# Performance work log

Hardware: AMD Instinct MI355X
Metric: run time of the kernel (lower is better)

The kernel has to match this reference:

```python
import jax, jax.numpy as jnp
import numpy as np

L_ITERS = 8   # number of ReduNet layers
C = 10        # number of classes
D = 1024      # feature dimension
N = 4096      # number of samples (columns of Z)


def setup_inputs() -> dict:
    key = jax.random.key(0)
    k0, k1, k2, k3 = jax.random.split(key, 4)
    Z = jax.random.normal(k0, (D, N), dtype=jnp.float32)
    # column-normalized features, as the net maintains at every layer
    Z = Z / jnp.linalg.norm(Z, axis=0, keepdims=True)
    # Elist[l]: (D,D) expansion operator; Cslist[l]: (C,D,D) per-class compression operators
    Elist = jax.random.normal(k1, (L_ITERS, D, D), dtype=jnp.float32) / np.float32(np.sqrt(D))
    Cslist = jax.random.normal(k2, (L_ITERS, C, D, D), dtype=jnp.float32) / np.float32(np.sqrt(D))
    gamma = jax.random.uniform(k3, (C,), dtype=jnp.float32)
    gamma = gamma / jnp.sum(gamma)
    eta = jnp.asarray(0.5, dtype=jnp.float32)
    temperature = jnp.asarray(0.1, dtype=jnp.float32)
    return {"Z": Z, "Elist": Elist, "Cslist": Cslist, "gamma": gamma,
            "eta": eta, "temperature": temperature, "L": L_ITERS}


def reference(Z, Elist, Cslist, gamma, eta, temperature, L):
    for l in range(L):
        Cs = Cslist[l]                                   # (C, d, d)
        CZ = jnp.einsum('cij,jn->cin', Cs, Z)            # (C, d, n)
        sims = -jnp.sqrt(jnp.sum(CZ * CZ, axis=1))       # fro norm over dim=1 -> (C, n)
        P_hat = jax.nn.softmax(sims / temperature, axis=0)  # softmax over classes
        PZ = P_hat[:, None, :] * Z                       # (C, d, n)
        term = jnp.einsum('c,cij,cjn->in', gamma, Cs, PZ)   # gamma-weighted class compression
        grads = Elist[l] @ Z - term                      # (d, n)
        Z = Z + eta * grads
        Z = Z / jnp.linalg.norm(Z, axis=0, keepdims=True)   # column-wise normalization
    return Z
```

## Files before the change

### kernel.cpp

```cpp
#include <hip/hip_runtime.h>
#include <hip/hip_bf16.h>
#include <stdint.h>

#define D_DIM 1024
#define N_DIM 4096
#define C_CLS 10
#define L_IT 8
#define M_DIM 11264
#define NBM 44

typedef __bf16 bf16_t;
typedef __bf16 bf16x8 __attribute__((ext_vector_type(8)));
typedef __bf16 bf16x4 __attribute__((ext_vector_type(4)));
typedef float  f32x4  __attribute__((ext_vector_type(4)));
typedef unsigned short u16x8 __attribute__((ext_vector_type(8)));

__device__ __forceinline__ float bf2f(uint16_t u) {
  union { uint32_t i; float f; } x; x.i = ((uint32_t)u) << 16; return x.f;
}

__global__ __launch_bounds__(256) void pack_w(const float4* __restrict__ Cs,
                                              const float4* __restrict__ El,
                                              bf16x4* __restrict__ dst) {
  const int CS4 = C_CLS * D_DIM * D_DIM / 4;
  int i = blockIdx.x * 256 + threadIdx.x;
  float4 v = (i < CS4) ? Cs[i] : El[i - CS4];
  bf16x4 o;
  o[0] = (bf16_t)v.x; o[1] = (bf16_t)v.y; o[2] = (bf16_t)v.z; o[3] = (bf16_t)v.w;
  dst[i] = o;
}

__global__ __launch_bounds__(256) void init_zt(const float* __restrict__ Zin,
                                               float* __restrict__ ZfT,
                                               bf16_t* __restrict__ ZbT) {
  __shared__ float tile[32][33];
  int tx = threadIdx.x & 31, ty = threadIdx.x >> 5;
  int nb = blockIdx.x, db = blockIdx.y;
  int n = nb * 32 + tx;
#pragma unroll
  for (int j = 0; j < 32; j += 8) {
    int d = db * 32 + ty + j;
    tile[ty + j][tx] = Zin[(size_t)d * N_DIM + n];
  }
  __syncthreads();
  int d2 = db * 32 + tx;
#pragma unroll
  for (int j = 0; j < 32; j += 8) {
    int n2 = nb * 32 + ty + j;
    float v = tile[tx][ty + j];
    ZfT[(size_t)n2 * D_DIM + d2] = v;
    ZbT[(size_t)n2 * D_DIM + d2] = (bf16_t)v;
  }
}

__global__ __launch_bounds__(256) void final_out(const float* __restrict__ ZfT,
                                                 float* __restrict__ outp) {
  __shared__ float tile[32][33];
  int tx = threadIdx.x & 31, ty = threadIdx.x >> 5;
  int nb = blockIdx.x, db = blockIdx.y;
#pragma unroll
  for (int j = 0; j < 32; j += 8) {
    int n = nb * 32 + ty + j;
    int d = db * 32 + tx;
    tile[ty + j][tx] = ZfT[(size_t)n * D_DIM + d];
  }
  __syncthreads();
#pragma unroll
  for (int j = 0; j < 32; j += 8) {
    int d2 = db * 32 + ty + j;
    int n2 = nb * 32 + tx;
    outp[(size_t)d2 * N_DIM + n2] = tile[tx][ty + j];
  }
}


#define SA(buf, h, t) do {                                                              \
    _Pragma("unroll") for (int e_ = 0; e_ < 2; ++e_) {                                  \
      const bf16_t* s_ = Wb + aoff0[e_] + (size_t)(h) * 65536 + (size_t)(t) * 64;       \
      __builtin_amdgcn_global_load_lds(                                                 \
        (const __attribute__((address_space(1))) void*)s_,                              \
        (__attribute__((address_space(3))) void*)(lds + (buf)*16384 + (h)*8192 + dstslot[e_]), \
        16, 0, 0);                                                                      \
    } } while (0)

#define SBst(buf, h, t) do {                                                            \
    _Pragma("unroll") for (int e_ = 0; e_ < 2; ++e_) {                                  \
      const bf16_t* s_ = ZbT + boff0[e_] + (size_t)(h) * 32768 + (size_t)(t) * 64;      \
      __builtin_amdgcn_global_load_lds(                                                 \
        (const __attribute__((address_space(1))) void*)s_,                              \
        (__attribute__((address_space(3))) void*)(lds + 32768 + (buf)*16384 + (h)*8192 + dstslot[e_]), \
        16, 0, 0);                                                                      \
    } } while (0)

#define LOAD_A(buf, qm) do {                                                            \
    _Pragma("unroll") for (int f_ = 0; f_ < 4; ++f_)                                    \
      _Pragma("unroll") for (int kk_ = 0; kk_ < 2; ++kk_)                               \
        a[f_][kk_] = *(const bf16x8*)(lds + (buf)*16384 + (qm)*8192 + aRowBase + f_*1024 + sidx[kk_]); \
  } while (0)

#define LOAD_Bq(buf, qn, arr) do {                                                      \
    _Pragma("unroll") for (int f_ = 0; f_ < 2; ++f_)                                    \
      _Pragma("unroll") for (int kk_ = 0; kk_ < 2; ++kk_)                               \
        arr[f_][kk_] = *(const bf16x8*)(lds + 32768 + (buf)*16384 + (qn)*8192 + bRowBase + f_*1024 + sidx[kk_]); \
  } while (0)

#define MFMAQ(qm, qn, arr) do {                                                         \
    _Pragma("unroll") for (int mm_ = 0; mm_ < 4; ++mm_)                                 \
      _Pragma("unroll") for (int nn_ = 0; nn_ < 2; ++nn_)                               \
        _Pragma("unroll") for (int kk_ = 0; kk_ < 2; ++kk_)                             \
          acc[(qm)*4+mm_][(qn)*2+nn_] = __builtin_amdgcn_mfma_f32_16x16x32_bf16(        \
            a[mm_][kk_], arr[nn_][kk_], acc[(qm)*4+mm_][(qn)*2+nn_], 0, 0, 0);          \
  } while (0)

#define BAR   __builtin_amdgcn_s_barrier()
#define VM(n) asm volatile("s_waitcnt vmcnt(" #n ")" ::: "memory")
#define PRIO1 __builtin_amdgcn_s_setprio(1)
#define PRIO0 __builtin_amdgcn_s_setprio(0)

#define PH(qm, LOADS, STAGES, WAIT) do {                                                \
    LOADS;                                                                              \
    STAGES;                                                                             \
    BAR;                                                                                \
    PRIO1;                                                                              \
    MFMAQ(qm, 0, b0);                                                                   \
    MFMAQ(qm, 1, b1);                                                                   \
    PRIO0;                                                                              \
    WAIT;                                                                               \
    BAR;                                                                                \
  } while (0)

__global__ __launch_bounds__(512, 2) void gemm_wz8(const bf16_t* __restrict__ Wb,
                                                   const bf16_t* __restrict__ ZbT,
                                                   bf16_t* __restrict__ OUT_T, int ldn,
                                                   float* __restrict__ ssq) {
  __shared__ __align__(16) bf16_t lds[65536];

  int nwg = gridDim.x;
  int bid = blockIdx.x;
  int q = nwg >> 3, r = nwg & 7;
  int xcd = bid & 7, idx = bid >> 3;
  int swz = (xcd < r ? xcd * (q + 1) : r * (q + 1) + (xcd - r) * q) + idx;
  int bm = swz % NBM, bn = swz / NBM;
  int m0 = bm * 256, n0 = bn * 256;

  int tid = threadIdx.x;
  int wave = tid >> 6, lane = tid & 63;
  int wrow = wave >> 2, wcol = wave & 3;
  int lm = lane & 15, lks = lane >> 4;
  int sw = lm & 7;

  size_t aoff0[2], boff0[2];
  int dstslot[2];
#pragma unroll
  for (int e = 0; e < 2; ++e) {
    int j = e * 512 + tid;
    int rih = j >> 3, sl = j & 7;
    int sg = sl ^ (rih & 7);
    int arow = (rih & 63) + ((rih >> 6) << 7);
    int brow = (rih & 31) + ((rih >> 5) << 6);
    aoff0[e] = (size_t)(m0 + arow) * 1024 + sg * 8;
    boff0[e] = (size_t)(n0 + brow) * 1024 + sg * 8;
    dstslot[e] = e * 4096 + wave * 512;
  }

  int aRowBase = (wrow * 64 + lm) * 64;
  int bRowBase = (wcol * 32 + lm) * 64;
  int sidx[2] = { ((0 + lks) ^ sw) * 8, ((4 + lks) ^ sw) * 8 };

  f32x4 acc[8][4] = {};
  bf16x8 a[4][2], b0[2][2], b1[2][2];

  SA(0, 0, 0); SBst(0, 0, 0); SBst(0, 1, 0);
  SA(0, 1, 0);
  SA(1, 0, 1); SBst(1, 0, 1); SBst(1, 1, 1);
  VM(8);
  BAR;

  for (int it = 0; it < 8; ++it) {
    int tO = 2 * it + 1, tN = 2 * it + 2, tM = 2 * it + 3;
    bool st = (it < 7);

    PH(0,
       LOAD_A(0, 0); LOAD_Bq(0, 0, b0); LOAD_Bq(0, 1, b1),
       SA(1, 1, tO),
       VM(8));

    if (st) {
      PH(1, LOAD_A(0, 1), SA(0, 0, tN); SBst(0, 0, tN); SBst(0, 1, tN), VM(8));
    } else {
      PH(1, LOAD_A(0, 1), , VM(2));
    }

    if (st) {
      PH(0, LOAD_A(1, 0); LOAD_Bq(1, 0, b0); LOAD_Bq(1, 1, b1), SA(0, 1, tN), VM(8));
    } else {
      PH(0, LOAD_A(1, 0); LOAD_Bq(1, 0, b0); LOAD_Bq(1, 1, b1), , VM(0));
    }

    if (st) {
      PH(1, LOAD_A(1, 1), SA(1, 0, tM); SBst(1, 0, tM); SBst(1, 1, tM), VM(8));
    } else {
      PH(1, LOAD_A(1, 1), , );
    }
  }

#pragma unroll
  for (int mf = 0; mf < 8; ++mf)
#pragma unroll
    for (int nf = 0; nf < 4; ++nf) {
      int col = n0 + wcol * 64 + nf * 16 + lm;
      int row = m0 + wrow * 128 + mf * 16 + lks * 4;
      bf16x4 v;
#pragma unroll
      for (int rr = 0; rr < 4; ++rr) v[rr] = (bf16_t)acc[mf][nf][rr];
      *(bf16x4*)(OUT_T + (size_t)col * M_DIM + row) = v;
    }

  if (m0 < C_CLS * 1024) {
    int c = m0 >> 10;
#pragma unroll
    for (int nf = 0; nf < 4; ++nf) {
      float v = 0.f;
#pragma unroll
      for (int mf = 0; mf < 8; ++mf)
#pragma unroll
        for (int rr = 0; rr < 4; ++rr)
          v += acc[mf][nf][rr] * acc[mf][nf][rr];
      v += __shfl_xor(v, 16);
      v += __shfl_xor(v, 32);
      if (lks == 0)
        atomicAdd(&ssq[(size_t)c * ldn + n0 + wcol * 64 + nf * 16 + lm], v);
    }
  }
}

__global__ __launch_bounds__(256) void update2(const bf16_t* __restrict__ OUT_T, int Nc,
                                               const float* __restrict__ ssq,
                                               const float* __restrict__ gamma,
                                               const float* __restrict__ etap,
                                               const float* __restrict__ tempr,
                                               float* __restrict__ ZfT,
                                               bf16_t* __restrict__ ZbT,
                                               int n_off) {
  int wv = threadIdx.x >> 6, lane = threadIdx.x & 63;
  int nl = blockIdx.x * 4 + wv;
  if (nl >= Nc) return;
  int n = n_off + nl;
  float eta = etap[0], invT = 1.0f / tempr[0];

  float s[C_CLS], m = -1e30f;
#pragma unroll
  for (int c = 0; c < C_CLS; ++c) {
    float sim = -sqrtf(ssq[(size_t)c * Nc + nl]);
    s[c] = sim;
    m = fmaxf(m, sim);
  }
  float sum = 0.f;
#pragma unroll
  for (int c = 0; c < C_CLS; ++c) {
    float e = __expf((s[c] - m) * invT);
    s[c] = e;
    sum += e;
  }
  float invsum = 1.0f / sum;
  float gP[C_CLS];
#pragma unroll
  for (int c = 0; c < C_CLS; ++c) gP[c] = gamma[c] * s[c] * invsum;

  const u16x8* ob = (const u16x8*)(OUT_T + (size_t)nl * M_DIM) + lane * 2;
  float term[16] = {};
#pragma unroll
  for (int c = 0; c < C_CLS; ++c) {
    u16x8 v0 = ob[c * 128], v1 = ob[c * 128 + 1];
#pragma unroll
    for (int j = 0; j < 8; ++j) {
      term[j]     += gP[c] * bf2f(v0[j]);
      term[8 + j] += gP[c] * bf2f(v1[j]);
    }
  }
  u16x8 g0 = ob[C_CLS * 128], g1 = ob[C_CLS * 128 + 1];

  const f32x4* zp = (const f32x4*)(ZfT + (size_t)n * D_DIM) + lane * 4;
  f32x4 z[4] = { zp[0], zp[1], zp[2], zp[3] };

  float zn[16];
  float ss = 0.f;
#pragma unroll
  for (int j = 0; j < 16; ++j) {
    float g = bf2f(j < 8 ? g0[j & 7] : g1[j & 7]);
    float v = z[j >> 2][j & 3] + eta * (g - term[j]);
    zn[j] = v;
    ss += v * v;
  }
#pragma unroll
  for (int k = 1; k < 64; k <<= 1) ss += __shfl_xor(ss, k);
  float inv = rsqrtf(ss);

  f32x4* zo = (f32x4*)(ZfT + (size_t)n * D_DIM) + lane * 4;
  bf16x8* bo = (bf16x8*)(ZbT + (size_t)n * D_DIM) + lane * 2;
#pragma unroll
  for (int q4 = 0; q4 < 4; ++q4) {
    f32x4 o;
#pragma unroll
    for (int j = 0; j < 4; ++j) o[j] = zn[q4 * 4 + j] * inv;
    zo[q4] = o;
  }
#pragma unroll
  for (int h = 0; h < 2; ++h) {
    bf16x8 o;
#pragma unroll
    for (int j = 0; j < 8; ++j) o[j] = (bf16_t)(zn[h * 8 + j] * inv);
    bo[h] = o;
  }
}

extern "C" void kernel_launch(void* const* d_in, const int* in_sizes, int n_in,
                              void* d_out, int out_size, void* d_ws, size_t ws_size,
                              hipStream_t stream) {
  (void)in_sizes; (void)n_in; (void)out_size;
  const float* Zin        = (const float*)d_in[0];
  const float* Elist      = (const float*)d_in[1];
  const float* Cslist     = (const float*)d_in[2];
  const float* gamma      = (const float*)d_in[3];
  const float* eta        = (const float*)d_in[4];
  const float* temperature= (const float*)d_in[5];

  auto align256 = [](size_t x) { return (x + 255) & ~(size_t)255; };
  size_t zbt_b = align256((size_t)N_DIM * D_DIM * 2);
  size_t zft_b = align256((size_t)N_DIM * D_DIM * 4);
  size_t wb_b  = align256((size_t)M_DIM * D_DIM * 2);
  size_t ssq_b = align256((size_t)L_IT * C_CLS * N_DIM * 4);
  size_t out_b = align256((size_t)M_DIM * N_DIM * 2);

  if (zbt_b + zft_b + wb_b + ssq_b + out_b > ws_size) {
    hipMemsetAsync(d_out, 0, (size_t)D_DIM * N_DIM * 4, stream);
    return;
  }

  char* p = (char*)d_ws;
  bf16_t* ZbT  = (bf16_t*)p; p += zbt_b;
  float*  ZfT  = (float*)p;  p += zft_b;
  bf16_t* Wb   = (bf16_t*)p; p += wb_b;
  float*  ssq  = (float*)p;  p += ssq_b;
  bf16_t* OUT_T= (bf16_t*)p;

  hipMemsetAsync(ssq, 0, (size_t)L_IT * C_CLS * N_DIM * 4, stream);
  init_zt<<<dim3(N_DIM / 32, D_DIM / 32), 256, 0, stream>>>(Zin, ZfT, ZbT);

  for (int l = 0; l < L_IT; ++l) {
    const float* Cs = Cslist + (size_t)l * C_CLS * D_DIM * D_DIM;
    const float* El = Elist  + (size_t)l * D_DIM * D_DIM;
    float* ssq_l = ssq + (size_t)l * C_CLS * N_DIM;

    pack_w<<<dim3(M_DIM * D_DIM / 4 / 256), 256, 0, stream>>>(
        (const float4*)Cs, (const float4*)El, (bf16x4*)Wb);

    gemm_wz8<<<dim3(NBM * (N_DIM / 256)), 512, 0, stream>>>(
        Wb, ZbT, OUT_T, N_DIM, ssq_l);
    update2<<<dim3(N_DIM / 4), 256, 0, stream>>>(
        OUT_T, N_DIM, ssq_l, gamma, eta, temperature, ZfT, ZbT, 0);
  }
  final_out<<<dim3(N_DIM / 32, D_DIM / 32), 256, 0, stream>>>(ZfT, (float*)d_out);
}
```

Measured before the change: 1.258 ms.

## Split GEMM main loop into eight finer phases with explicit lgkmcnt waits

Restructures the pipelined bf16 MFMA main loop from four phases per iteration into eight, each issuing one quarter of MFMAs and interleaving smaller LDS reads and global-to-LDS stages. Explicit lgkmcnt waits and adjusted vmcnt thresholds replace the coarser waits, aiming to spread memory traffic more evenly across compute and shrink stalls. The cost is twice as many workgroup barriers per iteration, and the hand-tuned wait counts risk races if they are wrong.

New measurement: 1.244 ms. About the same (-1.1%).

```diff
diff --git a/kernel.cpp b/kernel.cpp
--- a/kernel.cpp
+++ b/kernel.cpp
@@ -114,18 +114,21 @@
 
 #define BAR   __builtin_amdgcn_s_barrier()
 #define VM(n) asm volatile("s_waitcnt vmcnt(" #n ")" ::: "memory")
+#define LGKM8 asm volatile("s_waitcnt lgkmcnt(8)" ::: "memory")
+#define LGKM0 asm volatile("s_waitcnt lgkmcnt(0)" ::: "memory")
 #define PRIO1 __builtin_amdgcn_s_setprio(1)
 #define PRIO0 __builtin_amdgcn_s_setprio(0)
 
-#define PH(qm, LOADS, STAGES, WAIT) do {                                                \
+#define PH8(qm, qn, arr, LOADS, STAGES, PREBAR, POSTMFMA) do {                          \
     LOADS;                                                                              \
     STAGES;                                                                             \
+    PREBAR;                                                                             \
     BAR;                                                                                \
+    LGKM0;                                                                              \
     PRIO1;                                                                              \
-    MFMAQ(qm, 0, b0);                                                                   \
-    MFMAQ(qm, 1, b1);                                                                   \
+    MFMAQ(qm, qn, arr);                                                                 \
     PRIO0;                                                                              \
-    WAIT;                                                                               \
+    POSTMFMA;                                                                           \
     BAR;                                                                                \
   } while (0)
 
@@ -170,38 +173,24 @@
   f32x4 acc[8][4] = {};
   bf16x8 a[4][2], b0[2][2], b1[2][2];
 
-  SA(0, 0, 0); SBst(0, 0, 0); SBst(0, 1, 0);
-  SA(0, 1, 0);
+  SA(0, 0, 0); SBst(0, 0, 0); SBst(0, 1, 0); SA(0, 1, 0);
   SA(1, 0, 1); SBst(1, 0, 1); SBst(1, 1, 1);
-  VM(8);
+  VM(6);
   BAR;
 
   for (int it = 0; it < 8; ++it) {
     int tO = 2 * it + 1, tN = 2 * it + 2, tM = 2 * it + 3;
     bool st = (it < 7);
 
-    PH(0,
-       LOAD_A(0, 0); LOAD_Bq(0, 0, b0); LOAD_Bq(0, 1, b1),
-       SA(1, 1, tO),
-       VM(8));
-
-    if (st) {
-      PH(1, LOAD_A(0, 1), SA(0, 0, tN); SBst(0, 0, tN); SBst(0, 1, tN), VM(8));
-    } else {
-      PH(1, LOAD_A(0, 1), , VM(2));
-    }
-
-    if (st) {
-      PH(0, LOAD_A(1, 0); LOAD_Bq(1, 0, b0); LOAD_Bq(1, 1, b1), SA(0, 1, tN), VM(8));
-    } else {
-      PH(0, LOAD_A(1, 0); LOAD_Bq(1, 0, b0); LOAD_Bq(1, 1, b1), , VM(0));
-    }
-
-    if (st) {
-      PH(1, LOAD_A(1, 1), SA(1, 0, tM); SBst(1, 0, tM); SBst(1, 1, tM), VM(8));
-    } else {
-      PH(1, LOAD_A(1, 1), , );
-    }
+    PH8(0, 0, b0, LOAD_A(0, 0); LOAD_Bq(0, 0, b0), SA(1, 1, tO), LGKM8, );
+    PH8(0, 1, b1, LOAD_Bq(0, 1, b1), { if (st) SA(0, 0, tN); }, , );
+    PH8(1, 0, b0, LOAD_A(0, 1), { if (st) SBst(0, 0, tN); }, , );
+    PH8(1, 1, b1, , { if (st) SBst(0, 1, tN); }, ,
+        { if (st) { VM(6); } else { VM(0); } });
+    PH8(0, 0, b0, LOAD_A(1, 0); LOAD_Bq(1, 0, b0), { if (st) SA(0, 1, tN); }, LGKM8, );
+    PH8(0, 1, b1, LOAD_Bq(1, 1, b1), { if (st) SA(1, 0, tM); }, , );
+    PH8(1, 0, b0, LOAD_A(1, 1), { if (st) SBst(1, 0, tM); }, , );
+    PH8(1, 1, b1, , { if (st) SBst(1, 1, tM); }, , { if (st) VM(6); });
   }
 
 #pragma unroll
```
